# Performance work log

Hardware: AMD Instinct MI355X
Metric: run time of the kernel (lower is better)

## Reference

```python
import jax, jax.numpy as jnp
import numpy as np

N_HEADS, N_LEVELS, N_POINTS = 8, 4, 4


def _sample_bilinear(feat_flat, H, W, x, y):
    """feat_flat: [B, H*W, nH, hd]; x,y: [B,Q,nH,P] pixel coords (align_corners=False).
    Zero padding outside. Returns [B,Q,nH,P,hd]."""
    x0 = jnp.floor(x); y0 = jnp.floor(y)
    wx = x - x0; wy = y - y0                       # bilinear weights
    x0i = x0.astype(jnp.int32); y0i = y0.astype(jnp.int32)

    def gather(ix, iy):
        valid = ((ix >= 0) & (ix < W) & (iy >= 0) & (iy < H)).astype(feat_flat.dtype)
        idx = jnp.clip(iy, 0, H - 1) * W + jnp.clip(ix, 0, W - 1)
        B, Q, nH, P = idx.shape
        hd = feat_flat.shape[-1]
        idx2 = idx.transpose(0, 1, 3, 2).reshape(B, Q * P, nH)[..., None]
        v = jnp.take_along_axis(feat_flat, idx2, axis=1)       # [B,Q*P,nH,hd]
        v = v.reshape(B, Q, P, nH, hd).transpose(0, 1, 3, 2, 4)  # [B,Q,nH,P,hd]
        return v * valid[..., None]

    v00 = gather(x0i, y0i); v01 = gather(x0i + 1, y0i)
    v10 = gather(x0i, y0i + 1); v11 = gather(x0i + 1, y0i + 1)
    wxe = wx[..., None]; wye = wy[..., None]
    return (v00 * (1 - wxe) + v01 * wxe) * (1 - wye) + (v10 * (1 - wxe) + v11 * wxe) * wye


def setup_inputs() -> dict:
    key = jax.random.key(0)
    ks = jax.random.split(key, 10)
    B, C = 2, 256
    shapes = np.array([[128, 128], [64, 64], [32, 32], [16, 16]], dtype=np.int64)
    lens = shapes[:, 0] * shapes[:, 1]
    Len = int(lens.sum())  # 21760
    lsi = np.concatenate([[0], np.cumsum(lens)[:-1]])
    return {
        "query": jax.random.normal(ks[0], (B, Len, C), jnp.float32),
        "reference_points": jax.random.uniform(ks[1], (B, Len, 2), dtype=jnp.float32),
        "input_flatten": jax.random.normal(ks[2], (B, Len, C), jnp.float32),
        "spatial_shapes": jnp.asarray(shapes),
        "level_start_index": jnp.asarray(lsi),
        "W_off": jax.random.normal(ks[3], (C, N_HEADS * N_LEVELS * N_POINTS * 2), jnp.float32) * 0.01,
        "b_off": jax.random.normal(ks[4], (N_HEADS * N_LEVELS * N_POINTS * 2,), jnp.float32) * 0.01,
        "W_attn": jax.random.normal(ks[5], (C, N_HEADS * N_LEVELS * N_POINTS), jnp.float32) * 0.02,
        "b_attn": jax.random.normal(ks[6], (N_HEADS * N_LEVELS * N_POINTS,), jnp.float32) * 0.02,
        "W_out": jax.random.normal(ks[7], (C, C), jnp.float32) * 0.02,
        "b_out": jax.random.normal(ks[8], (C,), jnp.float32) * 0.02,
    }


def reference(query, reference_points, input_flatten, spatial_shapes, level_start_index,
              W_off, b_off, W_attn, b_attn, W_out, b_out):
    B, Q, C = query.shape
    nH, nL, nP = N_HEADS, N_LEVELS, N_POINTS
    hd = C // nH

    off = (query @ W_off + b_off).reshape(B, Q, nH, nL, nP, 2)
    aw = jax.nn.softmax((query @ W_attn + b_attn).reshape(B, Q, nH, nL * nP), axis=-1)
    aw = aw.reshape(B, Q, nH, nL, nP)

    shapes = np.asarray(spatial_shapes)                     # static (H,W) per level
    normalizer = jnp.asarray(np.stack([shapes[:, 1], shapes[:, 0]], -1), query.dtype)  # (W,H)
    loc = reference_points[:, :, None, None, None, :] + off / normalizer[None, None, None, :, None, :]

    starts = np.concatenate([[0], np.cumsum(shapes[:, 0] * shapes[:, 1])])
    out = jnp.zeros((B, Q, nH, hd), query.dtype)
    for lvl in range(nL):
        H, W = int(shapes[lvl, 0]), int(shapes[lvl, 1])
        feat = input_flatten[:, int(starts[lvl]):int(starts[lvl + 1]), :].reshape(B, H * W, nH, hd)
        l = loc[:, :, :, lvl, :, :]                          # [B,Q,nH,P,2]
        # grid_sample align_corners=False: pixel = ((2*loc-1)+1)/2*size - 0.5 = loc*size - 0.5
        x = l[..., 0] * W - 0.5
        y = l[..., 1] * H - 0.5
        sampled = _sample_bilinear(feat, H, W, x, y)         # [B,Q,nH,P,hd]
        out = out + (sampled * aw[:, :, :, lvl, :, None]).sum(axis=3)

    return out.reshape(B, Q, C) @ W_out + b_out
```

## Files before the change

kernel.cpp:

```cpp
#include <hip/hip_runtime.h>


#define NH 8
#define NL 4
#define NP 4
#define CDIM 256
#define HD 32
#define QB 16
#define QSTR 264
#define ASTR 132

typedef short bf16x8 __attribute__((ext_vector_type(8)));
typedef float f32x4  __attribute__((ext_vector_type(4)));
typedef _Float16 f16x8v __attribute__((ext_vector_type(8)));
typedef _Float16 f16x4v __attribute__((ext_vector_type(4)));
typedef _Float16 f16x2v __attribute__((ext_vector_type(2)));

#define SPLAT8(x) (f16x8v){(x),(x),(x),(x),(x),(x),(x),(x)}

__device__ __forceinline__ short f2bf(float x) {
    union { float f; unsigned u; } v; v.f = x;
    const unsigned r = v.u + 0x7FFFu + ((v.u >> 16) & 1u);
    return (short)(r >> 16);
}

__constant__ int LVL_S_C[4] = {0, 16384, 20480, 21504};

__global__ __launch_bounds__(256) void convert_all(
    const float* __restrict__ W_off, const float* __restrict__ W_attn,
    const float* __restrict__ W_out, const float* __restrict__ feat,
    short* __restrict__ wt, _Float16* __restrict__ fh, int n4)
{
    const int bid = blockIdx.x;
    if (bid < 640) {
        const int gid = bid * 256 + threadIdx.x;
        if (gid < 65536) {
            const int c = gid >> 8, k = gid & 255;
            wt[gid] = f2bf(W_off[k * 256 + c]);
        } else if (gid < 98304) {
            const int g = gid - 65536, c = g >> 8, k = g & 255;
            wt[gid] = f2bf(W_attn[k * 128 + c]);
        } else if (gid < 163840) {
            const int g = gid - 98304, c = g >> 8, k = g & 255;
            wt[gid] = f2bf(W_out[k * 256 + c]);
        }
    } else {
        const int gid = (bid - 640) * 256 + threadIdx.x;
        if (gid < n4) {
            const float4 v = *(const float4*)&feat[gid * 4];
            f16x4v o;
            o[0] = (_Float16)v.x; o[1] = (_Float16)v.y;
            o[2] = (_Float16)v.z; o[3] = (_Float16)v.w;
            *(f16x4v*)&fh[gid * 4] = o;
        }
    }
}

__global__ __launch_bounds__(256, 5) void msda_mega(
    const float* __restrict__ query, const float* __restrict__ ref_pts,
    const _Float16* __restrict__ feath, const short* __restrict__ wt,
    const float* __restrict__ b_off, const float* __restrict__ b_attn,
    const float* __restrict__ b_out, float* __restrict__ out, int Len)
{
    const int t = threadIdx.x;
    const int lane = t & 63;
    const int wave = t >> 6;
    const int qr = lane & 15;
    const int quad = lane >> 4;
    const long long qbase = (long long)blockIdx.x * QB;
    const int b = (int)(qbase / Len);

    __shared__ __align__(16) short uni[QB * CDIM];
    short* qp = uni;
    _Float16* offs16 = (_Float16*)uni;
    __shared__ float aw_lds[QB * 128];
    __shared__ __align__(16) short pre_lds[QB * CDIM];
    __shared__ float ref_sm[QB][2];

    #pragma unroll
    for (int it = 0; it < 4; ++it) {
        const int e = it * 1024 + t * 4;
        const int i = e >> 8, k = e & 255;
        const float4 v = *(const float4*)&query[(qbase + i) * CDIM + k];
        const int chunk = (k >> 5) * 64 + ((k >> 3) & 3) * 16 + i;
        short4 o;
        o.x = f2bf(v.x); o.y = f2bf(v.y); o.z = f2bf(v.z); o.w = f2bf(v.w);
        *(short4*)&qp[chunk * 8 + (k & 7)] = o;
    }
    if (t < QB * 2) ref_sm[t >> 1][t & 1] = ref_pts[(qbase + (t >> 1)) * 2 + (t & 1)];
    __syncthreads();

    const short* __restrict__ Wt_off  = wt;
    const short* __restrict__ Wt_attn = wt + 65536;
    const short* __restrict__ Wt_out  = wt + 98304;

    {
        f32x4 acc[4], acca[2];
        #pragma unroll
        for (int j = 0; j < 4; ++j) acc[j] = (f32x4){0.f, 0.f, 0.f, 0.f};
        #pragma unroll
        for (int j = 0; j < 2; ++j) acca[j] = (f32x4){0.f, 0.f, 0.f, 0.f};

        const short* bb_off  = Wt_off  + qr * 256 + quad * 8;
        const short* bb_attn = Wt_attn + qr * 256 + quad * 8;
        #pragma unroll
        for (int s = 0; s < 8; ++s) {
            const bf16x8 af = *(const bf16x8*)&qp[(s * 64 + lane) * 8];
            #pragma unroll
            for (int j = 0; j < 4; ++j) {
                const bf16x8 bf = *(const bf16x8*)(bb_off + ((j * 4 + wave) * 16) * 256 + s * 32);
                acc[j] = __builtin_amdgcn_mfma_f32_16x16x32_bf16(af, bf, acc[j], 0, 0, 0);
            }
            #pragma unroll
            for (int j = 0; j < 2; ++j) {
                const bf16x8 bf = *(const bf16x8*)(bb_attn + ((j * 4 + wave) * 16) * 256 + s * 32);
                acca[j] = __builtin_amdgcn_mfma_f32_16x16x32_bf16(af, bf, acca[j], 0, 0, 0);
            }
        }
        __syncthreads();

        #pragma unroll
        for (int j = 0; j < 4; ++j) {
            const int col = (j * 4 + wave) * 16 + qr;
            const float bo = b_off[col];
            const int h = col >> 5, rem = col & 31;
            const int pos = (rem >> 1) * 16 + h * 2 + (rem & 1);
            #pragma unroll
            for (int r = 0; r < 4; ++r)
                offs16[(quad * 4 + r) * 256 + pos] = (_Float16)(acc[j][r] + bo);
        }
        #pragma unroll
        for (int j = 0; j < 2; ++j) {
            const int col = (j * 4 + wave) * 16 + qr;
            const float ba = b_attn[col];
            const int h = col >> 4, rem = col & 15;
            #pragma unroll
            for (int r = 0; r < 4; ++r)
                aw_lds[(quad * 4 + r) * 128 + rem * 8 + h] = acca[j][r] + ba;
        }
    }
    __syncthreads();

    if (t < QB * NH) {
        const int i = t >> 3, h = t & 7;
        float* row = &aw_lds[i * 128];
        float vals[16], mx = -1e30f;
        #pragma unroll
        for (int j = 0; j < 16; ++j) { vals[j] = row[j * 8 + h]; mx = fmaxf(mx, vals[j]); }
        float s = 0.f;
        #pragma unroll
        for (int j = 0; j < 16; ++j) { vals[j] = __expf(vals[j] - mx); s += vals[j]; }
        const float inv = 1.f / s;
        #pragma unroll
        for (int j = 0; j < 16; ++j) row[j * 8 + h] = vals[j] * inv;
    }
    __syncthreads();

    {
        const int rl = t >> 5;
        const int l32 = t & 31;
        const int h = l32 >> 2, ct = l32 & 3;
        const int c0 = h * HD + ct * 8;
        #pragma unroll 1
        for (int pass = 0; pass < 2; ++pass) {
            const int i = pass * 8 + rl;
            const float rx = ref_sm[i][0], ry = ref_sm[i][1];
            const _Float16* __restrict__ offr = &offs16[i * 256 + h * 2];
            const float* __restrict__ awr = &aw_lds[i * 128 + h];
            float acc[8];
            #pragma unroll
            for (int c = 0; c < 8; ++c) acc[c] = 0.f;
            f16x8v p00, p01, p10, p11;
            float q00 = 0.f, q01 = 0.f, q10 = 0.f, q11 = 0.f;
            #pragma unroll
            for (int pi = 0; pi < 16; ++pi) {
                const int l = pi >> 2;
                const int Wl = 128 >> l;
                const int base = (b * Len + LVL_S_C[l]) * CDIM + c0;
                const f16x2v oxy = *(const f16x2v*)(offr + pi * 16);
                const float a = awr[pi * 8];
                const float x = fmaf(rx, (float)Wl, (float)oxy[0]) - 0.5f;
                const float y = fmaf(ry, (float)Wl, (float)oxy[1]) - 0.5f;
                const float xf = floorf(x), yf = floorf(y);
                const int x0 = (int)xf, y0 = (int)yf;
                const float wx = x - xf, wy = y - yf;
                const float ax0 = ((unsigned)x0       < (unsigned)Wl) ? (1.f - wx) : 0.f;
                const float ax1 = ((unsigned)(x0 + 1) < (unsigned)Wl) ? wx         : 0.f;
                const float ay0 = (((unsigned)y0       < (unsigned)Wl) ? (1.f - wy) : 0.f) * a;
                const float ay1 = (((unsigned)(y0 + 1) < (unsigned)Wl) ? wy         : 0.f) * a;
                const int x0c = min(max(x0, 0), Wl - 1), x1c = min(max(x0 + 1, 0), Wl - 1);
                const int y0c = min(max(y0, 0), Wl - 1), y1c = min(max(y0 + 1, 0), Wl - 1);
                const int r00 = base + (y0c * Wl + x0c) * CDIM;
                const int r01 = base + (y0c * Wl + x1c) * CDIM;
                const int r10 = base + (y1c * Wl + x0c) * CDIM;
                const int r11 = base + (y1c * Wl + x1c) * CDIM;
                const f16x8v n00 = *(const f16x8v*)(feath + r00);
                const f16x8v n01 = *(const f16x8v*)(feath + r01);
                const f16x8v n10 = *(const f16x8v*)(feath + r10);
                const f16x8v n11 = *(const f16x8v*)(feath + r11);
                if (pi > 0) {
                    f16x8v bil = p00 * SPLAT8((_Float16)q00);
                    bil += p01 * SPLAT8((_Float16)q01);
                    bil += p10 * SPLAT8((_Float16)q10);
                    bil += p11 * SPLAT8((_Float16)q11);
                    #pragma unroll
                    for (int c = 0; c < 8; ++c) acc[c] += (float)bil[c];
                }
                p00 = n00; p01 = n01; p10 = n10; p11 = n11;
                q00 = ax0 * ay0; q01 = ax1 * ay0; q10 = ax0 * ay1; q11 = ax1 * ay1;
            }
            {
                f16x8v bil = p00 * SPLAT8((_Float16)q00);
                bil += p01 * SPLAT8((_Float16)q01);
                bil += p10 * SPLAT8((_Float16)q10);
                bil += p11 * SPLAT8((_Float16)q11);
                #pragma unroll
                for (int c = 0; c < 8; ++c) acc[c] += (float)bil[c];
            }
            bf16x8 pv;
            #pragma unroll
            for (int c = 0; c < 8; ++c) pv[c] = f2bf(acc[c]);
            *(bf16x8*)&pre_lds[(h * 64 + ct * 16 + i) * 8] = pv;
        }
    }
    __syncthreads();

    {
        f32x4 acc[4];
        #pragma unroll
        for (int j = 0; j < 4; ++j) acc[j] = (f32x4){0.f, 0.f, 0.f, 0.f};
        const short* bb = Wt_out + qr * 256 + quad * 8;
        #pragma unroll
        for (int s = 0; s < 8; ++s) {
            const bf16x8 af = *(const bf16x8*)&pre_lds[(s * 64 + lane) * 8];
            #pragma unroll
            for (int j = 0; j < 4; ++j) {
                const bf16x8 bf = *(const bf16x8*)(bb + ((j * 4 + wave) * 16) * 256 + s * 32);
                acc[j] = __builtin_amdgcn_mfma_f32_16x16x32_bf16(af, bf, acc[j], 0, 0, 0);
            }
        }
        #pragma unroll
        for (int j = 0; j < 4; ++j) {
            const int col = (j * 4 + wave) * 16 + qr;
            const float bo = b_out[col];
            #pragma unroll
            for (int r = 0; r < 4; ++r)
                out[(qbase + quad * 4 + r) * CDIM + col] = acc[j][r] + bo;
        }
    }
}

__global__ __launch_bounds__(256) void msda_fused_fb(
    const float* __restrict__ query, const float* __restrict__ ref_pts,
    const float* __restrict__ feat_f32, const short* __restrict__ wt,
    const float* __restrict__ b_off, const float* __restrict__ b_attn,
    const float* __restrict__ b_out, float* __restrict__ out, int Len)
{
    const int t = threadIdx.x;
    const int lane = t & 63;
    const int wave = t >> 6;
    const int qr = lane & 15;
    const int quad = lane >> 4;
    const long long qbase = (long long)blockIdx.x * QB;
    const int b = (int)(qbase / Len);

    __shared__ __align__(16) char uni[QB * QSTR * 4];
    short* qp = (short*)uni;
    float* offs_lds = (float*)uni;
    __shared__ float aw_lds[QB * ASTR];
    __shared__ __align__(16) short pre_lds[QB * QSTR];
    __shared__ float ref_sm[QB][2];

    #pragma unroll
    for (int it = 0; it < 4; ++it) {
        const int e = it * 1024 + t * 4;
        const int i = e >> 8, k = e & 255;
        const float4 v = *(const float4*)&query[(qbase + i) * CDIM + k];
        short4 o;
        o.x = f2bf(v.x); o.y = f2bf(v.y); o.z = f2bf(v.z); o.w = f2bf(v.w);
        *(short4*)&qp[i * QSTR + k] = o;
    }
    if (t < QB * 2) ref_sm[t >> 1][t & 1] = ref_pts[(qbase + (t >> 1)) * 2 + (t & 1)];
    __syncthreads();

    const short* __restrict__ Wt_off  = wt;
    const short* __restrict__ Wt_attn = wt + 65536;
    const short* __restrict__ Wt_out  = wt + 98304;

    {
        f32x4 acc[4], acca[2];
        #pragma unroll
        for (int j = 0; j < 4; ++j) acc[j] = (f32x4){0.f, 0.f, 0.f, 0.f};
        #pragma unroll
        for (int j = 0; j < 2; ++j) acca[j] = (f32x4){0.f, 0.f, 0.f, 0.f};
        const short* bb_off  = Wt_off  + qr * 256 + quad * 8;
        const short* bb_attn = Wt_attn + qr * 256 + quad * 8;
        #pragma unroll
        for (int s = 0; s < 8; ++s) {
            const bf16x8 af = *(const bf16x8*)&qp[qr * QSTR + s * 32 + quad * 8];
            #pragma unroll
            for (int j = 0; j < 4; ++j) {
                const bf16x8 bf = *(const bf16x8*)(bb_off + ((j * 4 + wave) * 16) * 256 + s * 32);
                acc[j] = __builtin_amdgcn_mfma_f32_16x16x32_bf16(af, bf, acc[j], 0, 0, 0);
            }
            #pragma unroll
            for (int j = 0; j < 2; ++j) {
                const bf16x8 bf = *(const bf16x8*)(bb_attn + ((j * 4 + wave) * 16) * 256 + s * 32);
                acca[j] = __builtin_amdgcn_mfma_f32_16x16x32_bf16(af, bf, acca[j], 0, 0, 0);
            }
        }
        __syncthreads();
        #pragma unroll
        for (int j = 0; j < 4; ++j) {
            const int col = (j * 4 + wave) * 16 + qr;
            const float bo = b_off[col];
            const int h = col >> 5, rem = col & 31;
            #pragma unroll
            for (int r = 0; r < 4; ++r)
                offs_lds[(quad * 4 + r) * QSTR + rem * 8 + h] = acc[j][r] + bo;
        }
        #pragma unroll
        for (int j = 0; j < 2; ++j) {
            const int col = (j * 4 + wave) * 16 + qr;
            const float ba = b_attn[col];
            const int h = col >> 4, rem = col & 15;
            #pragma unroll
            for (int r = 0; r < 4; ++r)
                aw_lds[(quad * 4 + r) * ASTR + rem * 8 + h] = acca[j][r] + ba;
        }
    }
    __syncthreads();

    if (t < QB * NH) {
        const int i = t >> 3, h = t & 7;
        float* row = &aw_lds[i * ASTR];
        float vals[16], mx = -1e30f;
        #pragma unroll
        for (int j = 0; j < 16; ++j) { vals[j] = row[j * 8 + h]; mx = fmaxf(mx, vals[j]); }
        float s = 0.f;
        #pragma unroll
        for (int j = 0; j < 16; ++j) { vals[j] = __expf(vals[j] - mx); s += vals[j]; }
        const float inv = 1.f / s;
        #pragma unroll
        for (int j = 0; j < 16; ++j) row[j * 8 + h] = vals[j] * inv;
    }
    __syncthreads();

    {
        const int rl = t >> 5;
        const int l32 = t & 31;
        const int h = l32 >> 2, ct = l32 & 3;
        const int c0 = h * HD + ct * 8;
        #pragma unroll 1
        for (int pass = 0; pass < 2; ++pass) {
            const int i = pass * 8 + rl;
            const float rx = ref_sm[i][0], ry = ref_sm[i][1];
            const float* __restrict__ offr = &offs_lds[i * QSTR];
            const float* __restrict__ awr  = &aw_lds[i * ASTR];
            float acc[8];
            #pragma unroll
            for (int c = 0; c < 8; ++c) acc[c] = 0.f;
            #pragma unroll
            for (int l = 0; l < NL; ++l) {
                const int Wl = 128 >> l;
                const int base = (b * Len + LVL_S_C[l]) * CDIM + c0;
                #pragma unroll 2
                for (int p = 0; p < NP; ++p) {
                    const int pi = l * 4 + p;
                    const float ox = offr[pi * 16 + h];
                    const float oy = offr[pi * 16 + 8 + h];
                    const float a  = awr[pi * 8 + h];
                    const float x = fmaf(rx, (float)Wl, ox) - 0.5f;
                    const float y = fmaf(ry, (float)Wl, oy) - 0.5f;
                    const float xf = floorf(x), yf = floorf(y);
                    const int x0 = (int)xf, y0 = (int)yf;
                    const float wx = x - xf, wy = y - yf;
                    const float ax0 = ((unsigned)x0       < (unsigned)Wl) ? (1.f - wx) : 0.f;
                    const float ax1 = ((unsigned)(x0 + 1) < (unsigned)Wl) ? wx         : 0.f;
                    const float ay0 = (((unsigned)y0       < (unsigned)Wl) ? (1.f - wy) : 0.f) * a;
                    const float ay1 = (((unsigned)(y0 + 1) < (unsigned)Wl) ? wy         : 0.f) * a;
                    const int x0c = min(max(x0, 0), Wl - 1), x1c = min(max(x0 + 1, 0), Wl - 1);
                    const int y0c = min(max(y0, 0), Wl - 1), y1c = min(max(y0 + 1, 0), Wl - 1);
                    const float w00 = ax0 * ay0, w01 = ax1 * ay0;
                    const float w10 = ax0 * ay1, w11 = ax1 * ay1;
                    const int r0 = base + (y0c * Wl + x0c) * CDIM;
                    const int r1 = base + (y0c * Wl + x1c) * CDIM;
                    const int r2 = base + (y1c * Wl + x0c) * CDIM;
                    const int r3 = base + (y1c * Wl + x1c) * CDIM;
                    f32x4 a0 = *(const f32x4*)(feat_f32 + r0);
                    f32x4 a1 = *(const f32x4*)(feat_f32 + r0 + 4);
                    f32x4 b0 = *(const f32x4*)(feat_f32 + r1);
                    f32x4 b1 = *(const f32x4*)(feat_f32 + r1 + 4);
                    f32x4 c0v = *(const f32x4*)(feat_f32 + r2);
                    f32x4 c1 = *(const f32x4*)(feat_f32 + r2 + 4);
                    f32x4 d0 = *(const f32x4*)(feat_f32 + r3);
                    f32x4 d1 = *(const f32x4*)(feat_f32 + r3 + 4);
                    #pragma unroll
                    for (int c = 0; c < 4; ++c) {
                        acc[c]     += w00*a0[c] + w01*b0[c] + w10*c0v[c] + w11*d0[c];
                        acc[c + 4] += w00*a1[c] + w01*b1[c] + w10*c1[c]  + w11*d1[c];
                    }
                }
            }
            bf16x8 pv;
            #pragma unroll
            for (int c = 0; c < 8; ++c) pv[c] = f2bf(acc[c]);
            *(bf16x8*)&pre_lds[i * QSTR + c0] = pv;
        }
    }
    __syncthreads();

    {
        f32x4 acc[4];
        #pragma unroll
        for (int j = 0; j < 4; ++j) acc[j] = (f32x4){0.f, 0.f, 0.f, 0.f};
        const short* bb = Wt_out + qr * 256 + quad * 8;
        #pragma unroll
        for (int s = 0; s < 8; ++s) {
            const bf16x8 af = *(const bf16x8*)&pre_lds[qr * QSTR + s * 32 + quad * 8];
            #pragma unroll
            for (int j = 0; j < 4; ++j) {
                const bf16x8 bf = *(const bf16x8*)(bb + ((j * 4 + wave) * 16) * 256 + s * 32);
                acc[j] = __builtin_amdgcn_mfma_f32_16x16x32_bf16(af, bf, acc[j], 0, 0, 0);
            }
        }
        #pragma unroll
        for (int j = 0; j < 4; ++j) {
            const int col = (j * 4 + wave) * 16 + qr;
            const float bo = b_out[col];
            #pragma unroll
            for (int r = 0; r < 4; ++r)
                out[(qbase + quad * 4 + r) * CDIM + col] = acc[j][r] + bo;
        }
    }
}

extern "C" void kernel_launch(void* const* d_in, const int* in_sizes, int n_in,
                              void* d_out, int out_size, void* d_ws, size_t ws_size,
                              hipStream_t stream) {
    const float* query   = (const float*)d_in[0];
    const float* ref_pts = (const float*)d_in[1];
    const float* feat    = (const float*)d_in[2];
    const float* W_off  = (const float*)d_in[5];
    const float* b_off  = (const float*)d_in[6];
    const float* W_attn = (const float*)d_in[7];
    const float* b_attn = (const float*)d_in[8];
    const float* W_out  = (const float*)d_in[9];
    const float* b_out  = (const float*)d_in[10];
    float* out = (float*)d_out;

    const int B = 2;
    const int Len = in_sizes[1] / (B * 2);
    const int rows = B * Len;
    const size_t feat_elems = (size_t)rows * CDIM;

    char* ws = (char*)d_ws;
    short* wt = (short*)ws;
    _Float16* feath = (_Float16*)(ws + 327680);
    const size_t need = 327680 + feat_elems * 2;

    if (ws_size >= need) {
        const int n4 = (int)(feat_elems / 4);
        const int fblocks = (n4 + 255) / 256;
        convert_all<<<640 + fblocks, 256, 0, stream>>>(W_off, W_attn, W_out, feat,
                                                       wt, feath, n4);
        msda_mega<<<rows / QB, 256, 0, stream>>>(query, ref_pts, feath, wt,
                                                 b_off, b_attn, b_out, out, Len);
    } else {
        convert_all<<<640, 256, 0, stream>>>(W_off, W_attn, W_out, feat,
                                             wt, (_Float16*)nullptr, 0);
        msda_fused_fb<<<rows / QB, 256, 0, stream>>>(query, ref_pts, feat, wt,
                                                     b_off, b_attn, b_out, out, Len);
    }
}
```

Measured before the change: 295.2 us.

## Double-buffer bilinear gathers and pad/swizzle LDS to cut bank conflicts

The sampling loop now keeps two sample points' gathers in flight, A and B, instead of one. This deepens software prefetching so global-load latency is better hidden. LDS rows for the offsets and attention weights are padded (strides 264 and 132), and the bf16 MFMA operand chunks in qp and pre_lds use an XOR swizzle to reduce bank conflicts. The cost is more registers under a launch bound of 5 waves, which could cause spills or lower occupancy, plus slightly more LDS.

New measurement: 324.8 us. 1.1x slower.

```diff
diff --git a/kernel.cpp b/kernel.cpp
--- a/kernel.cpp
+++ b/kernel.cpp
@@ -9,6 +9,9 @@
 #define QB 16
 #define QSTR 264
 #define ASTR 132
+#define OF_STR 264
+#define AW_STR 132
+#define SWZ(c) ((c) ^ ((((c) >> 4)) & 7))
 
 typedef short bf16x8 __attribute__((ext_vector_type(8)));
 typedef float f32x4  __attribute__((ext_vector_type(4)));
@@ -70,10 +73,10 @@
     const long long qbase = (long long)blockIdx.x * QB;
     const int b = (int)(qbase / Len);
 
-    __shared__ __align__(16) short uni[QB * CDIM];
+    __shared__ __align__(16) short uni[QB * OF_STR];
     short* qp = uni;
     _Float16* offs16 = (_Float16*)uni;
-    __shared__ float aw_lds[QB * 128];
+    __shared__ float aw_lds[QB * AW_STR];
     __shared__ __align__(16) short pre_lds[QB * CDIM];
     __shared__ float ref_sm[QB][2];
 
@@ -85,7 +88,7 @@
         const int chunk = (k >> 5) * 64 + ((k >> 3) & 3) * 16 + i;
         short4 o;
         o.x = f2bf(v.x); o.y = f2bf(v.y); o.z = f2bf(v.z); o.w = f2bf(v.w);
-        *(short4*)&qp[chunk * 8 + (k & 7)] = o;
+        *(short4*)&qp[SWZ(chunk) * 8 + (k & 7)] = o;
     }
     if (t < QB * 2) ref_sm[t >> 1][t & 1] = ref_pts[(qbase + (t >> 1)) * 2 + (t & 1)];
     __syncthreads();
@@ -105,7 +108,7 @@
         const short* bb_attn = Wt_attn + qr * 256 + quad * 8;
         #pragma unroll
         for (int s = 0; s < 8; ++s) {
-            const bf16x8 af = *(const bf16x8*)&qp[(s * 64 + lane) * 8];
+            const bf16x8 af = *(const bf16x8*)&qp[SWZ(s * 64 + lane) * 8];
             #pragma unroll
             for (int j = 0; j < 4; ++j) {
                 const bf16x8 bf = *(const bf16x8*)(bb_off + ((j * 4 + wave) * 16) * 256 + s * 32);
@@ -127,7 +130,7 @@
             const int pos = (rem >> 1) * 16 + h * 2 + (rem & 1);
             #pragma unroll
             for (int r = 0; r < 4; ++r)
-                offs16[(quad * 4 + r) * 256 + pos] = (_Float16)(acc[j][r] + bo);
+                offs16[(quad * 4 + r) * OF_STR + pos] = (_Float16)(acc[j][r] + bo);
         }
         #pragma unroll
         for (int j = 0; j < 2; ++j) {
@@ -136,14 +139,14 @@
             const int h = col >> 4, rem = col & 15;
             #pragma unroll
             for (int r = 0; r < 4; ++r)
-                aw_lds[(quad * 4 + r) * 128 + rem * 8 + h] = acca[j][r] + ba;
+                aw_lds[(quad * 4 + r) * AW_STR + rem * 8 + h] = acca[j][r] + ba;
         }
     }
     __syncthreads();
 
     if (t < QB * NH) {
         const int i = t >> 3, h = t & 7;
-        float* row = &aw_lds[i * 128];
+        float* row = &aw_lds[i * AW_STR];
         float vals[16], mx = -1e30f;
         #pragma unroll
         for (int j = 0; j < 16; ++j) { vals[j] = row[j * 8 + h]; mx = fmaxf(mx, vals[j]); }
@@ -165,62 +168,64 @@
         for (int pass = 0; pass < 2; ++pass) {
             const int i = pass * 8 + rl;
             const float rx = ref_sm[i][0], ry = ref_sm[i][1];
-            const _Float16* __restrict__ offr = &offs16[i * 256 + h * 2];
-            const float* __restrict__ awr = &aw_lds[i * 128 + h];
+            const _Float16* __restrict__ offr = &offs16[i * OF_STR + h * 2];
+            const float* __restrict__ awr = &aw_lds[i * AW_STR + h];
             float acc[8];
             #pragma unroll
             for (int c = 0; c < 8; ++c) acc[c] = 0.f;
-            f16x8v p00, p01, p10, p11;
-            float q00 = 0.f, q01 = 0.f, q10 = 0.f, q11 = 0.f;
-            #pragma unroll
-            for (int pi = 0; pi < 16; ++pi) {
-                const int l = pi >> 2;
-                const int Wl = 128 >> l;
-                const int base = (b * Len + LVL_S_C[l]) * CDIM + c0;
-                const f16x2v oxy = *(const f16x2v*)(offr + pi * 16);
-                const float a = awr[pi * 8];
-                const float x = fmaf(rx, (float)Wl, (float)oxy[0]) - 0.5f;
-                const float y = fmaf(ry, (float)Wl, (float)oxy[1]) - 0.5f;
-                const float xf = floorf(x), yf = floorf(y);
-                const int x0 = (int)xf, y0 = (int)yf;
-                const float wx = x - xf, wy = y - yf;
-                const float ax0 = ((unsigned)x0       < (unsigned)Wl) ? (1.f - wx) : 0.f;
-                const float ax1 = ((unsigned)(x0 + 1) < (unsigned)Wl) ? wx         : 0.f;
-                const float ay0 = (((unsigned)y0       < (unsigned)Wl) ? (1.f - wy) : 0.f) * a;
-                const float ay1 = (((unsigned)(y0 + 1) < (unsigned)Wl) ? wy         : 0.f) * a;
-                const int x0c = min(max(x0, 0), Wl - 1), x1c = min(max(x0 + 1, 0), Wl - 1);
-                const int y0c = min(max(y0, 0), Wl - 1), y1c = min(max(y0 + 1, 0), Wl - 1);
-                const int r00 = base + (y0c * Wl + x0c) * CDIM;
-                const int r01 = base + (y0c * Wl + x1c) * CDIM;
-                const int r10 = base + (y1c * Wl + x0c) * CDIM;
-                const int r11 = base + (y1c * Wl + x1c) * CDIM;
-                const f16x8v n00 = *(const f16x8v*)(feath + r00);
-                const f16x8v n01 = *(const f16x8v*)(feath + r01);
-                const f16x8v n10 = *(const f16x8v*)(feath + r10);
-                const f16x8v n11 = *(const f16x8v*)(feath + r11);
-                if (pi > 0) {
-                    f16x8v bil = p00 * SPLAT8((_Float16)q00);
-                    bil += p01 * SPLAT8((_Float16)q01);
-                    bil += p10 * SPLAT8((_Float16)q10);
-                    bil += p11 * SPLAT8((_Float16)q11);
-                    #pragma unroll
-                    for (int c = 0; c < 8; ++c) acc[c] += (float)bil[c];
-                }
-                p00 = n00; p01 = n01; p10 = n10; p11 = n11;
-                q00 = ax0 * ay0; q01 = ax1 * ay0; q10 = ax0 * ay1; q11 = ax1 * ay1;
-            }
-            {
-                f16x8v bil = p00 * SPLAT8((_Float16)q00);
-                bil += p01 * SPLAT8((_Float16)q01);
-                bil += p10 * SPLAT8((_Float16)q10);
-                bil += p11 * SPLAT8((_Float16)q11);
-                #pragma unroll
-                for (int c = 0; c < 8; ++c) acc[c] += (float)bil[c];
-            }
+            f16x8v pA0, pA1, pA2, pA3, pB0, pB1, pB2, pB3;
+            float qA0, qA1, qA2, qA3, qB0, qB1, qB2, qB3;
+
+#define MSDA_ISSUE(pi, P0, P1, P2, P3, Q0, Q1, Q2, Q3) do {                         \
+            const int l_ = (pi) >> 2;                                               \
+            const int Wl_ = 128 >> l_;                                              \
+            const int base_ = (b * Len + LVL_S_C[l_]) * CDIM + c0;                  \
+            const f16x2v oxy_ = *(const f16x2v*)(offr + (pi) * 16);                 \
+            const float a_ = awr[(pi) * 8];                                         \
+            const float x_ = fmaf(rx, (float)Wl_, (float)oxy_[0]) - 0.5f;           \
+            const float y_ = fmaf(ry, (float)Wl_, (float)oxy_[1]) - 0.5f;           \
+            const float xf_ = floorf(x_), yf_ = floorf(y_);                         \
+            const int x0_ = (int)xf_, y0_ = (int)yf_;                               \
+            const float wx_ = x_ - xf_, wy_ = y_ - yf_;                             \
+            const float ax0_ = ((unsigned)x0_       < (unsigned)Wl_) ? (1.f - wx_) : 0.f; \
+            const float ax1_ = ((unsigned)(x0_ + 1) < (unsigned)Wl_) ? wx_         : 0.f; \
+            const float ay0_ = (((unsigned)y0_       < (unsigned)Wl_) ? (1.f - wy_) : 0.f) * a_; \
+            const float ay1_ = (((unsigned)(y0_ + 1) < (unsigned)Wl_) ? wy_         : 0.f) * a_; \
+            const int x0c_ = min(max(x0_, 0), Wl_ - 1), x1c_ = min(max(x0_ + 1, 0), Wl_ - 1); \
+            const int y0c_ = min(max(y0_, 0), Wl_ - 1), y1c_ = min(max(y0_ + 1, 0), Wl_ - 1); \
+            P0 = *(const f16x8v*)(feath + base_ + (y0c_ * Wl_ + x0c_) * CDIM);      \
+            P1 = *(const f16x8v*)(feath + base_ + (y0c_ * Wl_ + x1c_) * CDIM);      \
+            P2 = *(const f16x8v*)(feath + base_ + (y1c_ * Wl_ + x0c_) * CDIM);      \
+            P3 = *(const f16x8v*)(feath + base_ + (y1c_ * Wl_ + x1c_) * CDIM);      \
+            Q0 = ax0_ * ay0_; Q1 = ax1_ * ay0_;                                     \
+            Q2 = ax0_ * ay1_; Q3 = ax1_ * ay1_; } while (0)
+
+#define MSDA_ACCUM(P0, P1, P2, P3, Q0, Q1, Q2, Q3) do {                             \
+            f16x8v bil_ = P0 * SPLAT8((_Float16)Q0);                                \
+            bil_ += P1 * SPLAT8((_Float16)Q1);                                      \
+            bil_ += P2 * SPLAT8((_Float16)Q2);                                      \
+            bil_ += P3 * SPLAT8((_Float16)Q3);                                      \
+            _Pragma("unroll")                                                       \
+            for (int c_ = 0; c_ < 8; ++c_) acc[c_] += (float)bil_[c_]; } while (0)
+
+            MSDA_ISSUE(0, pA0, pA1, pA2, pA3, qA0, qA1, qA2, qA3);
+            MSDA_ISSUE(1, pB0, pB1, pB2, pB3, qB0, qB1, qB2, qB3);
+            #pragma unroll
+            for (int pi = 2; pi < 16; pi += 2) {
+                MSDA_ACCUM(pA0, pA1, pA2, pA3, qA0, qA1, qA2, qA3);
+                MSDA_ISSUE(pi, pA0, pA1, pA2, pA3, qA0, qA1, qA2, qA3);
+                MSDA_ACCUM(pB0, pB1, pB2, pB3, qB0, qB1, qB2, qB3);
+                MSDA_ISSUE(pi + 1, pB0, pB1, pB2, pB3, qB0, qB1, qB2, qB3);
+            }
+            MSDA_ACCUM(pA0, pA1, pA2, pA3, qA0, qA1, qA2, qA3);
+            MSDA_ACCUM(pB0, pB1, pB2, pB3, qB0, qB1, qB2, qB3);
+#undef MSDA_ISSUE
+#undef MSDA_ACCUM
+
             bf16x8 pv;
             #pragma unroll
             for (int c = 0; c < 8; ++c) pv[c] = f2bf(acc[c]);
-            *(bf16x8*)&pre_lds[(h * 64 + ct * 16 + i) * 8] = pv;
+            *(bf16x8*)&pre_lds[SWZ(h * 64 + ct * 16 + i) * 8] = pv;
         }
     }
     __syncthreads();
@@ -232,7 +237,7 @@
         const short* bb = Wt_out + qr * 256 + quad * 8;
         #pragma unroll
         for (int s = 0; s < 8; ++s) {
-            const bf16x8 af = *(const bf16x8*)&pre_lds[(s * 64 + lane) * 8];
+            const bf16x8 af = *(const bf16x8*)&pre_lds[SWZ(s * 64 + lane) * 8];
             #pragma unroll
             for (int j = 0; j < 4; ++j) {
                 const bf16x8 bf = *(const bf16x8*)(bb + ((j * 4 + wave) * 16) * 256 + s * 32);
```

## Swizzle LDS layouts, store attention weights as fp16, raise occupancy bound

Applied to the files above, without the earlier changes.

Applies XOR swizzles to the shared-memory tiles for the query, offsets, attention weights and pre-projection values to reduce bank conflicts. Attention weights are stored as fp16 in a head-contiguous layout so the softmax can use vector loads. Reference points move from shared memory into registers. Minimum blocks per CU rises from 5 to 8, which caps registers per thread. That cap risks spills, and fp16 attention weights lose some precision.

New measurement: 371.9 us. +26.0%, slower.

```diff
diff --git a/kernel.cpp b/kernel.cpp
--- a/kernel.cpp
+++ b/kernel.cpp
@@ -9,6 +9,7 @@
 #define QB 16
 #define QSTR 264
 #define ASTR 132
+#define SWZ(c) ((c) ^ ((((c) >> 4)) & 7))
 
 typedef short bf16x8 __attribute__((ext_vector_type(8)));
 typedef float f32x4  __attribute__((ext_vector_type(4)));
@@ -56,7 +57,7 @@
     }
 }
 
-__global__ __launch_bounds__(256, 5) void msda_mega(
+__global__ __launch_bounds__(256, 8) void msda_mega(
     const float* __restrict__ query, const float* __restrict__ ref_pts,
     const _Float16* __restrict__ feath, const short* __restrict__ wt,
     const float* __restrict__ b_off, const float* __restrict__ b_attn,
@@ -73,9 +74,14 @@
     __shared__ __align__(16) short uni[QB * CDIM];
     short* qp = uni;
     _Float16* offs16 = (_Float16*)uni;
-    __shared__ float aw_lds[QB * 128];
+    __shared__ __align__(16) _Float16 aw_lds[QB * 128];
     __shared__ __align__(16) short pre_lds[QB * CDIM];
-    __shared__ float ref_sm[QB][2];
+
+    const int rl = t >> 5;
+    const float rx0 = ref_pts[(qbase + rl) * 2];
+    const float ry0 = ref_pts[(qbase + rl) * 2 + 1];
+    const float rx1 = ref_pts[(qbase + 8 + rl) * 2];
+    const float ry1 = ref_pts[(qbase + 8 + rl) * 2 + 1];
 
     #pragma unroll
     for (int it = 0; it < 4; ++it) {
@@ -85,9 +91,8 @@
         const int chunk = (k >> 5) * 64 + ((k >> 3) & 3) * 16 + i;
         short4 o;
         o.x = f2bf(v.x); o.y = f2bf(v.y); o.z = f2bf(v.z); o.w = f2bf(v.w);
-        *(short4*)&qp[chunk * 8 + (k & 7)] = o;
-    }
-    if (t < QB * 2) ref_sm[t >> 1][t & 1] = ref_pts[(qbase + (t >> 1)) * 2 + (t & 1)];
+        *(short4*)&qp[SWZ(chunk) * 8 + (k & 7)] = o;
+    }
     __syncthreads();
 
     const short* __restrict__ Wt_off  = wt;
@@ -105,7 +110,7 @@
         const short* bb_attn = Wt_attn + qr * 256 + quad * 8;
         #pragma unroll
         for (int s = 0; s < 8; ++s) {
-            const bf16x8 af = *(const bf16x8*)&qp[(s * 64 + lane) * 8];
+            const bf16x8 af = *(const bf16x8*)&qp[SWZ(s * 64 + lane) * 8];
             #pragma unroll
             for (int j = 0; j < 4; ++j) {
                 const bf16x8 bf = *(const bf16x8*)(bb_off + ((j * 4 + wave) * 16) * 256 + s * 32);
@@ -124,7 +129,7 @@
             const int col = (j * 4 + wave) * 16 + qr;
             const float bo = b_off[col];
             const int h = col >> 5, rem = col & 31;
-            const int pos = (rem >> 1) * 16 + h * 2 + (rem & 1);
+            const int pos = (rem >> 1) * 16 + ((h ^ quad) << 1) + (rem & 1);
             #pragma unroll
             for (int r = 0; r < 4; ++r)
                 offs16[(quad * 4 + r) * 256 + pos] = (_Float16)(acc[j][r] + bo);
@@ -133,40 +138,49 @@
         for (int j = 0; j < 2; ++j) {
             const int col = (j * 4 + wave) * 16 + qr;
             const float ba = b_attn[col];
-            const int h = col >> 4, rem = col & 15;
-            #pragma unroll
-            for (int r = 0; r < 4; ++r)
-                aw_lds[(quad * 4 + r) * 128 + rem * 8 + h] = acca[j][r] + ba;
+            const int h = col >> 4;
+            #pragma unroll
+            for (int r = 0; r < 4; ++r)
+                aw_lds[(quad * 4 + r) * 128 + ((h ^ quad) << 4) + qr] =
+                    (_Float16)(acca[j][r] + ba);
         }
     }
     __syncthreads();
 
     if (t < QB * NH) {
         const int i = t >> 3, h = t & 7;
-        float* row = &aw_lds[i * 128];
+        const int key = (i >> 2) & 3;
+        _Float16* row = &aw_lds[i * 128 + ((h ^ key) << 4)];
+        f16x8v v0 = *(const f16x8v*)row;
+        f16x8v v1 = *(const f16x8v*)(row + 8);
         float vals[16], mx = -1e30f;
         #pragma unroll
-        for (int j = 0; j < 16; ++j) { vals[j] = row[j * 8 + h]; mx = fmaxf(mx, vals[j]); }
+        for (int j = 0; j < 8; ++j) { vals[j] = (float)v0[j]; vals[8 + j] = (float)v1[j]; }
+        #pragma unroll
+        for (int j = 0; j < 16; ++j) mx = fmaxf(mx, vals[j]);
         float s = 0.f;
         #pragma unroll
         for (int j = 0; j < 16; ++j) { vals[j] = __expf(vals[j] - mx); s += vals[j]; }
         const float inv = 1.f / s;
         #pragma unroll
-        for (int j = 0; j < 16; ++j) row[j * 8 + h] = vals[j] * inv;
-    }
-    __syncthreads();
-
-    {
-        const int rl = t >> 5;
+        for (int j = 0; j < 8; ++j) { v0[j] = (_Float16)(vals[j] * inv); v1[j] = (_Float16)(vals[8 + j] * inv); }
+        *(f16x8v*)row = v0;
+        *(f16x8v*)(row + 8) = v1;
+    }
+    __syncthreads();
+
+    {
         const int l32 = t & 31;
         const int h = l32 >> 2, ct = l32 & 3;
         const int c0 = h * HD + ct * 8;
         #pragma unroll 1
         for (int pass = 0; pass < 2; ++pass) {
             const int i = pass * 8 + rl;
-            const float rx = ref_sm[i][0], ry = ref_sm[i][1];
-            const _Float16* __restrict__ offr = &offs16[i * 256 + h * 2];
-            const float* __restrict__ awr = &aw_lds[i * 128 + h];
+            const float rx = pass ? rx1 : rx0;
+            const float ry = pass ? ry1 : ry0;
+            const int key = (i >> 2) & 3;
+            const _Float16* __restrict__ offr = &offs16[i * 256 + ((h ^ key) << 1)];
+            const _Float16* __restrict__ awr  = &aw_lds[i * 128 + ((h ^ key) << 4)];
             float acc[8];
             #pragma unroll
             for (int c = 0; c < 8; ++c) acc[c] = 0.f;
@@ -178,7 +192,7 @@
                 const int Wl = 128 >> l;
                 const int base = (b * Len + LVL_S_C[l]) * CDIM + c0;
                 const f16x2v oxy = *(const f16x2v*)(offr + pi * 16);
-                const float a = awr[pi * 8];
+                const float a = (float)awr[pi];
                 const float x = fmaf(rx, (float)Wl, (float)oxy[0]) - 0.5f;
                 const float y = fmaf(ry, (float)Wl, (float)oxy[1]) - 0.5f;
                 const float xf = floorf(x), yf = floorf(y);
@@ -220,7 +234,7 @@
             bf16x8 pv;
             #pragma unroll
             for (int c = 0; c < 8; ++c) pv[c] = f2bf(acc[c]);
-            *(bf16x8*)&pre_lds[(h * 64 + ct * 16 + i) * 8] = pv;
+            *(bf16x8*)&pre_lds[SWZ(h * 64 + ct * 16 + i) * 8] = pv;
         }
     }
     __syncthreads();
@@ -232,7 +246,7 @@
         const short* bb = Wt_out + qr * 256 + quad * 8;
         #pragma unroll
         for (int s = 0; s < 8; ++s) {
-            const bf16x8 af = *(const bf16x8*)&pre_lds[(s * 64 + lane) * 8];
+            const bf16x8 af = *(const bf16x8*)&pre_lds[SWZ(s * 64 + lane) * 8];
             #pragma unroll
             for (int j = 0; j < 4; ++j) {
                 const bf16x8 bf = *(const bf16x8*)(bb + ((j * 4 + wave) * 16) * 256 + s * 32);
```
